# Kernel tuning notes

Measured on AMD Instinct MI355X. Metric: run time of the kernel, lower is better.

Reference implementation:

```python
import jax, jax.numpy as jnp
import numpy as np

N = 50000      # nodes per type
E = 800000     # edges per relation
CIN = 64       # in_channels
H, O = 2, 32   # heads, out_channels
HID = H * O    # hidden
EC = 16        # edge_channels


def setup_inputs() -> dict:
    key = jax.random.key(0)
    ks = jax.random.split(key, 30)
    f = lambda i, shape, s=0.1: jax.random.normal(ks[i], shape, dtype=jnp.float32) * s
    inp = {
        'x_a': f(0, (N, CIN), 1.0), 'x_b': f(1, (N, CIN), 1.0),
        'edge_attr1': f(2, (E, EC), 1.0), 'edge_attr2': f(3, (E, EC), 1.0),
        'Wq_a': f(4, (CIN, HID)), 'Wk_a': f(5, (CIN, HID)), 'Wv_a': f(6, (CIN, HID)),
        'Wq_b': f(7, (CIN, HID)), 'Wk_b': f(8, (CIN, HID)), 'Wv_b': f(9, (CIN, HID)),
        'emb_a': f(10, (HID,)), 'emb_b': f(11, (HID,)),
        'rel1': f(12, (HID,)), 'rel2': f(13, (HID,)),
        'We': f(14, (EC, HID)), 'a_attn': f(15, (4 * O,)),
        'Wo_a': f(16, (HID, O)), 'bo_a': f(17, (O,)),
        'Wo_b': f(18, (HID, O)), 'bo_b': f(19, (O,)),
        'Wr_a': f(20, (CIN, O)), 'Wr_b': f(21, (CIN, O)),
        'row1': jax.random.randint(ks[22], (E,), 0, N),
        'col1': jax.random.randint(ks[23], (E,), 0, N),
        'row2': jax.random.randint(ks[24], (E,), 0, N),
        'col2': jax.random.randint(ks[25], (E,), 0, N),
    }
    return inp


def _edge_softmax(scores, col, num_dst):
    # softmax over incoming edges of each destination node; scores: [E, H]
    m = jax.ops.segment_max(scores, col, num_segments=num_dst)      # [N, H]
    ex = jnp.exp(scores - m[col])
    s = jax.ops.segment_sum(ex, col, num_segments=num_dst)          # [N, H]
    return ex / s[col]


def _relation(q_dst, k_src, v_src, emb_src, emb_dst, rel_emb, edge_bias,
              row, col, a_attn, num_dst):
    eb = edge_bias                                                  # [E, H, O]
    qd = q_dst[col] + emb_dst.reshape(1, H, O)
    ks = k_src[row] + emb_src.reshape(1, H, O)
    rb = jnp.broadcast_to(rel_emb.reshape(1, H, O), qd.shape)
    attn_in = jnp.concatenate([qd, ks, rb, eb], axis=-1)            # [E, H, 4O]
    scores = jnp.einsum('ehd,d->eh', jnp.tanh(attn_in), a_attn)    # [E, H]
    w = _edge_softmax(scores, col, num_dst)                         # [E, H]
    msg = v_src[row] + rel_emb.reshape(1, H, O) + eb                # [E, H, O]
    agg = jax.ops.segment_sum(msg * w[..., None], col, num_segments=num_dst)
    return agg.reshape(num_dst, H * O)


def reference(x_a, x_b, edge_attr1, edge_attr2,
              Wq_a, Wk_a, Wv_a, Wq_b, Wk_b, Wv_b,
              emb_a, emb_b, rel1, rel2, We, a_attn,
              Wo_a, bo_a, Wo_b, bo_b, Wr_a, Wr_b,
              row1, col1, row2, col2):
    q_a = (x_a @ Wq_a).reshape(-1, H, O)
    k_a = (x_a @ Wk_a).reshape(-1, H, O)
    v_a = (x_a @ Wv_a).reshape(-1, H, O)
    q_b = (x_b @ Wq_b).reshape(-1, H, O)
    k_b = (x_b @ Wk_b).reshape(-1, H, O)
    v_b = (x_b @ Wv_b).reshape(-1, H, O)

    # relation r1: a -> b
    eb1 = (edge_attr1 @ We).reshape(-1, H, O)
    out_b = _relation(q_b, k_a, v_a, emb_a, emb_b, rel1, eb1, row1, col1, a_attn, N)
    # relation r2: b -> a
    eb2 = (edge_attr2 @ We).reshape(-1, H, O)
    out_a = _relation(q_a, k_b, v_b, emb_b, emb_a, rel2, eb2, row2, col2, a_attn, N)

    fin_a = out_a @ Wo_a + bo_a + x_a @ Wr_a                        # [N, O]
    fin_b = out_b @ Wo_b + bo_b + x_b @ Wr_b                        # [N, O]
    return jnp.concatenate([fin_a, fin_b], axis=0)                  # [2N, O]
```

## Files before the change

### kernel.cpp

```cpp
#include <hip/hip_runtime.h>
#include <hip/hip_bf16.h>

typedef __hip_bfloat16 bf16;
typedef __attribute__((ext_vector_type(8))) short short8;
typedef __attribute__((ext_vector_type(4))) float float4v;

static __device__ __forceinline__ float b2f(bf16 x) { return __bfloat162float(x); }

static __device__ __forceinline__ float ldf(const void* p, size_t i, int f32) {
    return f32 ? ((const float*)p)[i] : b2f(((const bf16*)p)[i]);
}
static __device__ __forceinline__ void stf(void* p, size_t i, int f32, float v) {
    if (f32) ((float*)p)[i] = v;
    else     ((bf16*)p)[i] = __float2bfloat16(v);
}
static __device__ __forceinline__ unsigned short f2bf_bits(float f) {
    bf16 h = __float2bfloat16(f);
    return *(unsigned short*)&h;
}

static __device__ __forceinline__ float fast_tanh(float x) {
    float t = __expf(2.f * x);
    return 1.f - 2.f * __builtin_amdgcn_rcpf(t + 1.f);
}

__global__ void detect_kernel(const unsigned short* __restrict__ a, int* __restrict__ flag)
{
    __shared__ int cnt;
    if (threadIdx.x == 0) cnt = 0;
    __syncthreads();
    unsigned e = (a[threadIdx.x] >> 7) & 0xFF;
    if (e < 100 || e > 133) atomicAdd(&cnt, 1);
    __syncthreads();
    if (threadIdx.x == 0) *flag = (cnt >= 16) ? 1 : 0;
}

__global__ __launch_bounds__(256) void prep_small_kernel(
    const void* __restrict__ W0, const void* __restrict__ W1,
    const void* __restrict__ W2, const void* __restrict__ W3,
    const void* __restrict__ W4, const void* __restrict__ W5,
    const void* __restrict__ Wr_a, const void* __restrict__ Wr_b,
    const void* __restrict__ We,
    const void* __restrict__ Wo_a, const void* __restrict__ Wo_b,
    const void* __restrict__ rel1, const void* __restrict__ rel2,
    const void* __restrict__ a_attn, const int* __restrict__ flagp,
    unsigned short* __restrict__ wt,
    float* __restrict__ M1, float* __restrict__ c321,
    float* __restrict__ M2, float* __restrict__ c322,
    float* __restrict__ cvals)
{
    const int f32 = *flagp;
    const int bid = blockIdx.x;
    if (bid < 6) {
        const void* src;
        switch (bid) {
            case 0: src = W0; break; case 1: src = W1; break; case 2: src = W2; break;
            case 3: src = W3; break; case 4: src = W4; break; default: src = W5; break;
        }
        unsigned short* dst = wt + bid * 4096;
        for (int i = threadIdx.x; i < 4096; i += 256) {
            int c = i >> 6, j = i & 63;
            dst[j * 64 + c] = f2bf_bits(ldf(src, c * 64 + j, f32));
        }
    } else if (bid < 8) {
        const void* src = (bid == 6) ? Wr_a : Wr_b;
        unsigned short* dst = wt + 24576 + (bid - 6) * 2048;
        for (int i = threadIdx.x; i < 2048; i += 256) {
            int c = i >> 5, j = i & 31;
            dst[j * 64 + c] = f2bf_bits(ldf(src, c * 32 + j, f32));
        }
    } else if (bid < 10) {
        const int sel = bid - 8;
        const void* Wo  = sel ? Wo_a : Wo_b;
        const void* rel = sel ? rel2 : rel1;
        float* M   = sel ? M2 : M1;
        float* c32 = sel ? c322 : c321;
        const int t = threadIdx.x;
        for (int i = t; i < 1024; i += 256) {
            int m = i >> 5, j = i & 31;
            int h = m >> 4, c = m & 15;
            float s = 0.f;
            for (int jj = 0; jj < 32; ++jj)
                s += ldf(We, c * 64 + h * 32 + jj, f32) * ldf(Wo, (size_t)(h * 32 + jj) * 32 + j, f32);
            M[m * 32 + j] = s;
        }
        if (t < 32) {
            float s2 = 0.f;
            for (int ch = 0; ch < 64; ++ch)
                s2 += ldf(rel, ch, f32) * ldf(Wo, (size_t)ch * 32 + t, f32);
            c32[t] = s2;
        }
        if (t == 252 || t == 253) {
            int h = t - 252;
            float s3 = 0.f;
            for (int l = 0; l < 32; ++l)
                s3 += tanhf(ldf(rel, h * 32 + l, f32)) * ldf(a_attn, 64 + l, f32);
            cvals[sel * 2 + h] = s3;
        }
    } else {
        unsigned short* wet = wt + 28672;
        for (int i = threadIdx.x; i < 1024; i += 256) {
            int n = i >> 4, k = i & 15;
            wet[n * 16 + k] = f2bf_bits(ldf(We, k * 64 + n, f32));
        }
    }
}

__global__ __launch_bounds__(256) void node_prep_mfma_kernel(
    const void* __restrict__ x_a, const void* __restrict__ x_b,
    const unsigned short* __restrict__ wt,
    const void* __restrict__ emb_a, const void* __restrict__ emb_b,
    const void* __restrict__ a_attn, const int* __restrict__ flagp,
    unsigned short* __restrict__ v_a, unsigned short* __restrict__ v_b,
    float* __restrict__ r_a, float* __restrict__ r_b,
    float* __restrict__ sq_a, float* __restrict__ sk_a,
    float* __restrict__ sq_b, float* __restrict__ sk_b,
    const int* __restrict__ col1, const int* __restrict__ col2,
    int* __restrict__ cnt, int* __restrict__ rank_out,
    int n_nodes, int tiles, int mfma_blocks, int num_e)
{
    const int f32 = *flagp;

    if ((int)blockIdx.x >= mfma_blocks) {
        const int hb  = blockIdx.x - mfma_blocks;
        const int sel = hb & 1;
        const int bx  = hb >> 1;
        const int* col = sel ? col2 : col1;
        const int rb = sel ? n_nodes : 0;
        int e = bx * 256 + threadIdx.x;
        if (e < num_e)
            rank_out[(size_t)sel * num_e + e] = atomicAdd(&cnt[rb + col[e]], 1);
        return;
    }

    const int wave_id = blockIdx.x * 4 + (threadIdx.x >> 6);
    if (wave_id >= 2 * tiles) return;
    const int type = (wave_id >= tiles);
    const int tile = type ? (wave_id - tiles) : wave_id;

    const void* xp = type ? x_b : x_a;
    const unsigned short* wq = wt + (type ? 3 * 4096 : 0);
    const unsigned short* wk = wq + 4096;
    const unsigned short* wv = wk + 4096;
    const unsigned short* wr = wt + 24576 + (type ? 2048 : 0);
    const void* embp = type ? emb_b : emb_a;
    unsigned short* v_out = type ? v_b : v_a;
    float*  r_out  = type ? r_b : r_a;
    float2* sq_out = (float2*)(type ? sq_b : sq_a);
    float2* sk_out = (float2*)(type ? sk_b : sk_a);

    const int lane = threadIdx.x & 63;
    const int ml   = lane & 15;
    const int g    = lane >> 4;
    const int g8   = g * 8;

    float embc[4], acq[4], ack[4];
    #pragma unroll
    for (int t = 0; t < 4; ++t) {
        int colt = t * 16 + ml;
        embc[t] = ldf(embp, colt, f32);
        acq[t]  = ldf(a_attn, colt & 31, f32);
        ack[t]  = ldf(a_attn, 32 + (colt & 31), f32);
    }

    short8 Bq[4][2], Bk[4][2], Bv[4][2], Br[2][2];
    #pragma unroll
    for (int t = 0; t < 4; ++t) {
        const int rowo = (t * 16 + ml) * 64;
        #pragma unroll
        for (int kh = 0; kh < 2; ++kh) {
            const int o = rowo + kh * 32 + g8;
            Bq[t][kh] = __builtin_bit_cast(short8, *(const uint4*)(wq + o));
            Bk[t][kh] = __builtin_bit_cast(short8, *(const uint4*)(wk + o));
            Bv[t][kh] = __builtin_bit_cast(short8, *(const uint4*)(wv + o));
            if (t < 2)
                Br[t][kh] = __builtin_bit_cast(short8, *(const uint4*)(wr + o));
        }
    }

    const int n0 = tile << 4;
    int nr = n0 + ml; if (nr > n_nodes - 1) nr = n_nodes - 1;
    short8 A0, A1;
    if (f32) {
        const float4* xr = (const float4*)((const float*)xp + (size_t)nr * 64);
        float4 f0 = xr[2*g], f1 = xr[2*g+1], f2 = xr[8+2*g], f3 = xr[9+2*g];
        short8 a0, a1;
        a0[0]=(short)f2bf_bits(f0.x); a0[1]=(short)f2bf_bits(f0.y);
        a0[2]=(short)f2bf_bits(f0.z); a0[3]=(short)f2bf_bits(f0.w);
        a0[4]=(short)f2bf_bits(f1.x); a0[5]=(short)f2bf_bits(f1.y);
        a0[6]=(short)f2bf_bits(f1.z); a0[7]=(short)f2bf_bits(f1.w);
        a1[0]=(short)f2bf_bits(f2.x); a1[1]=(short)f2bf_bits(f2.y);
        a1[2]=(short)f2bf_bits(f2.z); a1[3]=(short)f2bf_bits(f2.w);
        a1[4]=(short)f2bf_bits(f3.x); a1[5]=(short)f2bf_bits(f3.y);
        a1[6]=(short)f2bf_bits(f3.z); a1[7]=(short)f2bf_bits(f3.w);
        A0 = a0; A1 = a1;
    } else {
        const uint4* xr = (const uint4*)((const bf16*)xp + (size_t)nr * 64);
        A0 = __builtin_bit_cast(short8, xr[g]);
        A1 = __builtin_bit_cast(short8, xr[4 + g]);
    }

    float4v accq[4], acck[4], accv[4], accr[2];
    #pragma unroll
    for (int t = 0; t < 4; ++t) {
        float4v z = {0.f, 0.f, 0.f, 0.f};
        accq[t] = z; acck[t] = z; accv[t] = z;
        if (t < 2) accr[t] = z;
    }
    #pragma unroll
    for (int t = 0; t < 4; ++t) {
        accq[t] = __builtin_amdgcn_mfma_f32_16x16x32_bf16(A0, Bq[t][0], accq[t], 0, 0, 0);
        accq[t] = __builtin_amdgcn_mfma_f32_16x16x32_bf16(A1, Bq[t][1], accq[t], 0, 0, 0);
        acck[t] = __builtin_amdgcn_mfma_f32_16x16x32_bf16(A0, Bk[t][0], acck[t], 0, 0, 0);
        acck[t] = __builtin_amdgcn_mfma_f32_16x16x32_bf16(A1, Bk[t][1], acck[t], 0, 0, 0);
        accv[t] = __builtin_amdgcn_mfma_f32_16x16x32_bf16(A0, Bv[t][0], accv[t], 0, 0, 0);
        accv[t] = __builtin_amdgcn_mfma_f32_16x16x32_bf16(A1, Bv[t][1], accv[t], 0, 0, 0);
        if (t < 2) {
            accr[t] = __builtin_amdgcn_mfma_f32_16x16x32_bf16(A0, Br[t][0], accr[t], 0, 0, 0);
            accr[t] = __builtin_amdgcn_mfma_f32_16x16x32_bf16(A1, Br[t][1], accr[t], 0, 0, 0);
        }
    }

    #pragma unroll
    for (int t = 0; t < 4; ++t) {
        #pragma unroll
        for (int r = 0; r < 4; ++r) {
            int node = n0 + g * 4 + r;
            if (node < n_nodes) {
                v_out[(size_t)node * 64 + t * 16 + ml] = f2bf_bits(accv[t][r]);
                if (t < 2) r_out[(size_t)node * 32 + t * 16 + ml] = accr[t][r];
            }
        }
    }

    #pragma unroll
    for (int r = 0; r < 4; ++r) {
        float q0 = fast_tanh(accq[0][r] + embc[0]) * acq[0]
                 + fast_tanh(accq[1][r] + embc[1]) * acq[1];
        float q1 = fast_tanh(accq[2][r] + embc[2]) * acq[2]
                 + fast_tanh(accq[3][r] + embc[3]) * acq[3];
        float k0 = fast_tanh(acck[0][r] + embc[0]) * ack[0]
                 + fast_tanh(acck[1][r] + embc[1]) * ack[1];
        float k1 = fast_tanh(acck[2][r] + embc[2]) * ack[2]
                 + fast_tanh(acck[3][r] + embc[3]) * ack[3];
        #pragma unroll
        for (int o = 1; o < 16; o <<= 1) {
            q0 += __shfl_xor(q0, o, 64); q1 += __shfl_xor(q1, o, 64);
            k0 += __shfl_xor(k0, o, 64); k1 += __shfl_xor(k1, o, 64);
        }
        int node = n0 + g * 4 + r;
        if (ml == 0 && node < n_nodes) {
            sq_out[node] = make_float2(q0, q1);
            sk_out[node] = make_float2(k0, k1);
        }
    }
}

__global__ __launch_bounds__(256) void scan1_kernel(const int* __restrict__ cnt,
                                                    int* __restrict__ partial, int n)
{
    __shared__ int wsum[4];
    int t = threadIdx.x;
    int i0 = blockIdx.x * 512 + 2 * t;
    int s = ((i0 < n) ? cnt[i0] : 0) + ((i0 + 1 < n) ? cnt[i0 + 1] : 0);
    #pragma unroll
    for (int o = 32; o; o >>= 1) s += __shfl_xor(s, o, 64);
    if ((t & 63) == 0) wsum[t >> 6] = s;
    __syncthreads();
    if (t == 0) partial[blockIdx.x] = wsum[0] + wsum[1] + wsum[2] + wsum[3];
}

__global__ void scan2_kernel(const int* __restrict__ partial, int* __restrict__ pp,
                             int* __restrict__ off, int nch, int noff)
{
    int lane = threadIdx.x;
    int running = 0;
    for (int base = 0; base < nch; base += 64) {
        int i = base + lane;
        int o = (i < nch) ? partial[i] : 0;
        int v = o;
        #pragma unroll
        for (int d = 1; d < 64; d <<= 1) {
            int u = __shfl_up(v, d, 64);
            if (lane >= d) v += u;
        }
        if (i < nch) pp[i] = running + v - o;
        running += __shfl(v, 63, 64);
    }
    if (lane == 0) off[noff] = running;
}

__global__ __launch_bounds__(256) void scan3_kernel(const int* __restrict__ cnt,
                                                    const int* __restrict__ pp,
                                                    int* __restrict__ off, int n)
{
    __shared__ int tmp[256];
    int t = threadIdx.x;
    int i0 = blockIdx.x * 512 + 2 * t;
    int v0 = (i0 < n) ? cnt[i0] : 0;
    int v1 = (i0 + 1 < n) ? cnt[i0 + 1] : 0;
    int pair = v0 + v1;
    tmp[t] = pair;
    __syncthreads();
    for (int d = 1; d < 256; d <<= 1) {
        int x = (t >= d) ? tmp[t - d] : 0;
        __syncthreads();
        tmp[t] += x;
        __syncthreads();
    }
    int excl = tmp[t] - pair + pp[blockIdx.x];
    if (i0 < n)     off[i0] = excl;
    if (i0 + 1 < n) off[i0 + 1] = excl + v0;
}

__global__ __launch_bounds__(256) void edge_score_scatter_kernel(
    const void* __restrict__ ea1p, const void* __restrict__ ea2p,
    const unsigned short* __restrict__ wet,
    const int* __restrict__ row1, const int* __restrict__ col1,
    const int* __restrict__ row2, const int* __restrict__ col2,
    const float* __restrict__ sq_bp, const float* __restrict__ sk_ap,
    const float* __restrict__ sq_ap, const float* __restrict__ sk_bp,
    const float* __restrict__ cvals, const void* __restrict__ a_attn,
    const int* __restrict__ flagp,
    const int* __restrict__ offs, const int* __restrict__ rankp,
    uint4* __restrict__ payload, int n_nodes, int num_e)
{
    const int f32 = *flagp;
    const int sel = blockIdx.x & 1;
    const int bx  = blockIdx.x >> 1;
    const void* ea = sel ? ea2p : ea1p;
    const int* row = sel ? row2 : row1;
    const int* col = sel ? col2 : col1;
    const float* sq_dst = sel ? sq_ap : sq_bp;
    const float* sk_src = sel ? sk_bp : sk_ap;
    const int rb = sel ? n_nodes : 0;
    const int* rankr = rankp + (size_t)sel * num_e;

    const int lane = threadIdx.x & 63;
    const int wv   = threadIdx.x >> 6;
    const int ml   = lane & 15;
    const int g    = lane >> 4;
    const int rsel = lane & 3;

    const int base = bx * 256 + wv * 64;
    if (base >= num_e) return;

    const short8 zero8 = {0, 0, 0, 0, 0, 0, 0, 0};

    short8 B[4];
    #pragma unroll
    for (int t = 0; t < 4; ++t)
        B[t] = (g < 2) ? __builtin_bit_cast(short8, *(const uint4*)(wet + (t * 16 + ml) * 16 + g * 8))
                       : zero8;
    float av[4];
    #pragma unroll
    for (int t = 0; t < 4; ++t) av[t] = ldf(a_attn, 96 + ((t * 16 + ml) & 31), f32);
    const float c0 = cvals[sel * 2 + 0];
    const float c1 = cvals[sel * 2 + 1];

    int pcol[4]; unsigned psrc[4]; int prank[4];
    #pragma unroll
    for (int it = 0; it < 4; ++it) { pcol[it] = 0; psrc[it] = 0; prank[it] = 0; }
    if (ml < 4) {
        #pragma unroll
        for (int it = 0; it < 4; ++it) {
            int e = base + it * 16 + g * 4 + rsel;
            int ec = (e < num_e) ? e : (num_e - 1);
            pcol[it]  = col[ec];
            psrc[it]  = (unsigned)row[ec];
            prank[it] = rankr[ec];
        }
    }

    short8 A[4];
    #pragma unroll
    for (int it = 0; it < 4; ++it) {
        int ec = base + it * 16 + ml; if (ec > num_e - 1) ec = num_e - 1;
        if (g < 2) {
            if (f32) {
                const float4* p = (const float4*)((const float*)ea + (size_t)ec * 16 + g * 8);
                float4 f0 = p[0], f1 = p[1];
                short8 a;
                a[0] = (short)f2bf_bits(f0.x); a[1] = (short)f2bf_bits(f0.y);
                a[2] = (short)f2bf_bits(f0.z); a[3] = (short)f2bf_bits(f0.w);
                a[4] = (short)f2bf_bits(f1.x); a[5] = (short)f2bf_bits(f1.y);
                a[6] = (short)f2bf_bits(f1.z); a[7] = (short)f2bf_bits(f1.w);
                A[it] = a;
            } else {
                A[it] = __builtin_bit_cast(short8, *(const uint4*)((const bf16*)ea + (size_t)ec * 16 + g * 8));
            }
        } else {
            A[it] = zero8;
        }
    }

    int ppos[4]; float2 psq[4], psk[4];
    #pragma unroll
    for (int it = 0; it < 4; ++it) {
        ppos[it] = 0;
        psq[it] = make_float2(0.f, 0.f); psk[it] = make_float2(0.f, 0.f);
    }
    if (ml < 4) {
        #pragma unroll
        for (int it = 0; it < 4; ++it) {
            psq[it] = ((const float2*)sq_dst)[pcol[it]];
            psk[it] = ((const float2*)sk_src)[psrc[it]];
            ppos[it] = offs[rb + pcol[it]] + prank[it];
        }
    }

    #pragma unroll
    for (int it = 0; it < 4; ++it) {
        const int e0 = base + it * 16;
        if (e0 < num_e) {
            float4v z = {0.f, 0.f, 0.f, 0.f};
            float4v acc0 = z, acc1 = z, acc2 = z, acc3 = z;
            acc0 = __builtin_amdgcn_mfma_f32_16x16x32_bf16(A[it], B[0], acc0, 0, 0, 0);
            acc1 = __builtin_amdgcn_mfma_f32_16x16x32_bf16(A[it], B[1], acc1, 0, 0, 0);
            acc2 = __builtin_amdgcn_mfma_f32_16x16x32_bf16(A[it], B[2], acc2, 0, 0, 0);
            acc3 = __builtin_amdgcn_mfma_f32_16x16x32_bf16(A[it], B[3], acc3, 0, 0, 0);

            float s0[4], s1[4];
            #pragma unroll
            for (int r = 0; r < 4; ++r) {
                s0[r] = fast_tanh(acc0[r]) * av[0] + fast_tanh(acc1[r]) * av[1];
                s1[r] = fast_tanh(acc2[r]) * av[2] + fast_tanh(acc3[r]) * av[3];
            }
            #pragma unroll
            for (int o = 1; o < 16; o <<= 1) {
                #pragma unroll
                for (int r = 0; r < 4; ++r) {
                    s0[r] += __shfl_xor(s0[r], o, 64);
                    s1[r] += __shfl_xor(s1[r], o, 64);
                }
            }

            const bool fin = (ml < 4) && (e0 + g * 4 + rsel < num_e);
            if (fin) {
                float a0 = (rsel == 0) ? s0[0] : (rsel == 1) ? s0[1] : (rsel == 2) ? s0[2] : s0[3];
                float a1 = (rsel == 0) ? s1[0] : (rsel == 1) ? s1[1] : (rsel == 2) ? s1[2] : s1[3];
                float v0 = fminf(30.f, fmaxf(-30.f, a0 + psq[it].x + psk[it].x + c0));
                float v1 = fminf(30.f, fmaxf(-30.f, a1 + psq[it].y + psk[it].y + c1));
                uint4* rec = payload + (size_t)3 * ppos[it];
                rec[0] = make_uint4(psrc[it], __float_as_uint(__expf(v0)),
                                    __float_as_uint(__expf(v1)), 0u);
            }
            const int srcl = ((lane & 12) << 2) | (lane & 3);
            const int posx = __shfl(ppos[it], srcl, 64);
            if (lane < 32 && (e0 + ml < num_e)) {
                uint4* rec = payload + (size_t)3 * posx;
                rec[1 + g] = __builtin_bit_cast(uint4, A[it]);
            }
        }
    }
}

__global__ __launch_bounds__(256) void agg_final_kernel(
    const uint4* __restrict__ payload, const int* __restrict__ off,
    const unsigned short* __restrict__ v_a, const unsigned short* __restrict__ v_b,
    const float* __restrict__ r_a, const float* __restrict__ r_b,
    const void* __restrict__ Wo_a, const void* __restrict__ Wo_b,
    const void* __restrict__ bo_a, const void* __restrict__ bo_b,
    const float* __restrict__ M1, const float* __restrict__ M2,
    const float* __restrict__ c321, const float* __restrict__ c322,
    const int* __restrict__ flagp, void* __restrict__ out,
    int n_nodes, int nbh)
{
    const int sel = blockIdx.x & 1;
    const int bx  = blockIdx.x >> 1;
    const unsigned short* v_src = sel ? v_b : v_a;
    const float* r_src = sel ? r_a : r_b;
    const void*  Wo    = sel ? Wo_a : Wo_b;
    const void*  bo    = sel ? bo_a : bo_b;
    const float* M     = sel ? M2 : M1;
    const float* c32   = sel ? c322 : c321;
    const int relbase  = sel ? n_nodes : 0;
    const size_t out_off = sel ? 0 : (size_t)n_nodes * 32;

    const int f32  = *flagp;
    const int lane = threadIdx.x & 63;
    const int wv   = threadIdx.x >> 6;
    const int j    = lane & 31;
    const int half = lane >> 5;
    const int c16  = lane & 15;
    const bool hi  = (lane >= 32);

    __shared__ float stage[4][96];

    float WoR[32], MR[16];
    const int cb = half * 32;
    #pragma unroll
    for (int cc = 0; cc < 32; ++cc)
        WoR[cc] = ldf(Wo, (size_t)(cb + cc) * 32 + j, f32);
    const int ub = half * 16;
    #pragma unroll
    for (int cc = 0; cc < 16; ++cc) MR[cc] = M[(ub + cc) * 32 + j];
    const float boR  = ldf(bo, j, f32);
    const float c32R = c32[j];

    const int stride = nbh * 4;
    const int iters  = (n_nodes + stride - 1) / stride;
    int d = bx * 4 + wv;

    int dd0 = (d < n_nodes) ? d : (n_nodes - 1);
    int b_c  = off[relbase + dd0];
    int en_c = off[relbase + dd0 + 1];
    float rv_c = r_src[(size_t)dd0 * 32 + j];

    for (int it = 0; it < iters; ++it, d += stride) {
        const bool valid = (d < n_nodes);
        const int dd  = valid ? d : (n_nodes - 1);

        int b_n = 0, en_n = 0; float rv_n = 0.f;
        if (it + 1 < iters) {
            int dn  = d + stride;
            int ddn = (dn < n_nodes) ? dn : (n_nodes - 1);
            b_n  = off[relbase + ddn];
            en_n = off[relbase + ddn + 1];
            rv_n = r_src[(size_t)ddn * 32 + j];
        }

        const int b   = __builtin_amdgcn_readfirstlane(b_c);
        const int en  = __builtin_amdgcn_readfirstlane(en_c);
        const int deg = en - b;
        const float rv = rv_c;

        float den0 = 0.f, den1 = 0.f, y = 0.f, ua = 0.f;
        int k = b;
        #pragma unroll 1
        for (; k + 8 <= en; k += 8) {
            uint4 m[8];
            #pragma unroll
            for (int q = 0; q < 8; ++q) m[q] = payload[(size_t)3 * (k + q)];
            float ev[8];
            #pragma unroll
            for (int q = 0; q < 8; ++q) {
                const unsigned short* pq = (const unsigned short*)(payload + (size_t)3 * (k + q) + 1);
                ev[q] = __uint_as_float((unsigned)pq[c16] << 16);
            }
            float vv[8];
            #pragma unroll
            for (int q = 0; q < 8; ++q)
                vv[q] = __uint_as_float((unsigned)v_src[(size_t)m[q].x * 64 + lane] << 16);
            #pragma unroll
            for (int q = 0; q < 8; ++q) {
                float e0 = __uint_as_float(m[q].y), e1 = __uint_as_float(m[q].z);
                den0 += e0; den1 += e1;
                float xw = hi ? e1 : e0;
                y  = fmaf(xw, vv[q], y);
                ua = fmaf(xw, ev[q], ua);
            }
        }
        #pragma unroll 1
        for (; k < en; ++k) {
            uint4 mm = payload[(size_t)3 * k];
            const unsigned short* pq = (const unsigned short*)(payload + (size_t)3 * k + 1);
            float evs = __uint_as_float((unsigned)pq[c16] << 16);
            float vvs = __uint_as_float((unsigned)v_src[(size_t)mm.x * 64 + lane] << 16);
            float e0 = __uint_as_float(mm.y), e1 = __uint_as_float(mm.z);
            den0 += e0; den1 += e1;
            float xw = hi ? e1 : e0;
            y  = fmaf(xw, vvs, y);
            ua = fmaf(xw, evs, ua);
        }

        float inv0 = (deg > 0) ? __builtin_amdgcn_rcpf(den0) : 0.f;
        float inv1 = (deg > 0) ? __builtin_amdgcn_rcpf(den1) : 0.f;
        const float invh = hi ? inv1 : inv0;
        y  *= invh;
        ua *= invh;

        float* st = stage[wv];
        st[lane] = y;
        if ((lane & 31) < 16) st[64 + half * 16 + c16] = ua;
        __asm__ volatile("s_waitcnt lgkmcnt(0)" ::: "memory");

        float acc = 0.f;
        #pragma unroll
        for (int cc = 0; cc < 32; ++cc)
            acc = fmaf(st[cb + cc], WoR[cc], acc);
        #pragma unroll
        for (int cc = 0; cc < 16; ++cc)
            acc = fmaf(st[64 + ub + cc], MR[cc], acc);

        float other = __shfl(acc, lane ^ 32, 64);
        if (valid && lane < 32) {
            float o = acc + other + boR + rv + ((deg > 0) ? c32R : 0.f);
            stf(out, out_off + (size_t)dd * 32 + j, f32, o);
        }
        __asm__ volatile("" ::: "memory");
        __builtin_amdgcn_wave_barrier();

        b_c = b_n; en_c = en_n; rv_c = rv_n;
    }
}

extern "C" void kernel_launch(void* const* d_in, const int* in_sizes, int n_in,
                              void* d_out, int out_size, void* d_ws, size_t ws_size,
                              hipStream_t stream)
{
    const void* x_a   = d_in[0];
    const void* x_b   = d_in[1];
    const void* ea1   = d_in[2];
    const void* ea2   = d_in[3];
    const void* Wq_a  = d_in[4];
    const void* Wk_a  = d_in[5];
    const void* Wv_a  = d_in[6];
    const void* Wq_b  = d_in[7];
    const void* Wk_b  = d_in[8];
    const void* Wv_b  = d_in[9];
    const void* emb_a = d_in[10];
    const void* emb_b = d_in[11];
    const void* rel1  = d_in[12];
    const void* rel2  = d_in[13];
    const void* We    = d_in[14];
    const void* a_at  = d_in[15];
    const void* Wo_a  = d_in[16];
    const void* bo_a  = d_in[17];
    const void* Wo_b  = d_in[18];
    const void* bo_b  = d_in[19];
    const void* Wr_a  = d_in[20];
    const void* Wr_b  = d_in[21];
    const int*  row1  = (const int*)d_in[22];
    const int*  col1  = (const int*)d_in[23];
    const int*  row2  = (const int*)d_in[24];
    const int*  col2  = (const int*)d_in[25];

    const int N = in_sizes[0] / 64;
    const int E = in_sizes[22];

    float* ws = (float*)d_ws;
    size_t off = 0;
    int*   flag = (int*)ws;        off += 64;
    unsigned short* v_a = (unsigned short*)(ws + off); off += (size_t)N * 32;
    unsigned short* v_b = (unsigned short*)(ws + off); off += (size_t)N * 32;
    float* r_a  = ws + off;        off += (size_t)N * 32;
    float* r_b  = ws + off;        off += (size_t)N * 32;
    float* sq_a = ws + off;        off += (size_t)N * 2;
    float* sk_a = ws + off;        off += (size_t)N * 2;
    float* sq_b = ws + off;        off += (size_t)N * 2;
    float* sk_b = ws + off;        off += (size_t)N * 2;
    float* cvals = ws + off;       off += 4;
    off = (off + 3) & ~(size_t)3;
    unsigned short* wt = (unsigned short*)(ws + off); off += 29696 / 2;
    float* M1   = ws + off;        off += 1024;
    float* c321 = ws + off;        off += 32;
    float* M2   = ws + off;        off += 1024;
    float* c322 = ws + off;        off += 32;
    int*   cnt    = (int*)(ws + off);  off += (size_t)2 * N;
    int*   offs   = (int*)(ws + off);  off += (size_t)2 * N + 2;
    int*   rankp  = (int*)(ws + off);  off += (size_t)2 * E;
    int*   partial = (int*)(ws + off); off += 512;
    int*   pp      = (int*)(ws + off); off += 512;
    off = (off + 3) & ~(size_t)3;
    uint4* payload = (uint4*)(ws + off); off += (size_t)2 * E * 12;

    const int tiles        = (N + 15) >> 4;
    const int mfma_blocks  = (2 * tiles + 3) / 4;
    const int eb_blocks    = (E + 255) / 256;
    const int score_blocks = (E + 255) / 256;
    const int nch          = (2 * N + 511) / 512;
    const int agg_half     = 4096;

    detect_kernel<<<1, 128, 0, stream>>>((const unsigned short*)a_at, flag);
    hipMemsetAsync(cnt, 0, (size_t)2 * N * sizeof(int), stream);

    prep_small_kernel<<<11, 256, 0, stream>>>(
        Wq_a, Wk_a, Wv_a, Wq_b, Wk_b, Wv_b, Wr_a, Wr_b,
        We, Wo_a, Wo_b, rel1, rel2, a_at, flag,
        wt, M1, c321, M2, c322, cvals);

    node_prep_mfma_kernel<<<mfma_blocks + 2 * eb_blocks, 256, 0, stream>>>(
        x_a, x_b, wt, emb_a, emb_b, a_at, flag,
        v_a, v_b, r_a, r_b, sq_a, sk_a, sq_b, sk_b,
        col1, col2, cnt, rankp, N, tiles, mfma_blocks, E);

    scan1_kernel<<<nch, 256, 0, stream>>>(cnt, partial, 2 * N);
    scan2_kernel<<<1, 64, 0, stream>>>(partial, pp, offs, nch, 2 * N);
    scan3_kernel<<<nch, 256, 0, stream>>>(cnt, pp, offs, 2 * N);

    edge_score_scatter_kernel<<<2 * score_blocks, 256, 0, stream>>>(
        ea1, ea2, wt + 28672, row1, col1, row2, col2,
        sq_b, sk_a, sq_a, sk_b, cvals, a_at, flag,
        offs, rankp, payload, N, E);

    agg_final_kernel<<<2 * agg_half, 256, 0, stream>>>(
        payload, offs, v_a, v_b, r_a, r_b, Wo_a, Wo_b, bo_a, bo_b,
        M1, M2, c321, c322, flag, d_out, N, agg_half);
}
```

Measured before the change: 525.3 us.

## Pad edge payload records to 64 bytes and read them with coalesced lane-wide loads

Each per-edge payload record grows from 48 to 64 bytes and is written as four full uint4 slots by cooperating lanes using shuffles, instead of scattered partial writes. In the aggregation kernel a wavefront now reads four whole records with one coalesced dword-per-lane load and pulls the source index, exp weights and edge features out with cross-lane shuffles, replacing many small per-edge loads. The aggregation grid is also halved. The cost is more payload memory traffic from padding and extra shuffle instructions per edge.

```diff
diff --git a/kernel.cpp b/kernel.cpp
--- a/kernel.cpp
+++ b/kernel.cpp
@@ -435,22 +435,33 @@
                 }
             }
 
+            float ex0v = 0.f, ex1v = 0.f;
             const bool fin = (ml < 4) && (e0 + g * 4 + rsel < num_e);
             if (fin) {
                 float a0 = (rsel == 0) ? s0[0] : (rsel == 1) ? s0[1] : (rsel == 2) ? s0[2] : s0[3];
                 float a1 = (rsel == 0) ? s1[0] : (rsel == 1) ? s1[1] : (rsel == 2) ? s1[2] : s1[3];
                 float v0 = fminf(30.f, fmaxf(-30.f, a0 + psq[it].x + psk[it].x + c0));
                 float v1 = fminf(30.f, fmaxf(-30.f, a1 + psq[it].y + psk[it].y + c1));
-                uint4* rec = payload + (size_t)3 * ppos[it];
-                rec[0] = make_uint4(psrc[it], __float_as_uint(__expf(v0)),
-                                    __float_as_uint(__expf(v1)), 0u);
+                ex0v = __expf(v0); ex1v = __expf(v1);
             }
+
             const int srcl = ((lane & 12) << 2) | (lane & 3);
             const int posx = __shfl(ppos[it], srcl, 64);
-            if (lane < 32 && (e0 + ml < num_e)) {
-                uint4* rec = payload + (size_t)3 * posx;
-                rec[1 + g] = __builtin_bit_cast(uint4, A[it]);
-            }
+            const unsigned psx = (unsigned)__shfl((int)psrc[it], srcl, 64);
+            const float e0x = __shfl(ex0v, srcl, 64);
+            const float e1x = __shfl(ex1v, srcl, 64);
+            uint4 Au = __builtin_bit_cast(uint4, A[it]);
+            uint4 Ad;
+            Ad.x = (unsigned)__shfl((int)Au.x, lane - 16, 64);
+            Ad.y = (unsigned)__shfl((int)Au.y, lane - 16, 64);
+            Ad.z = (unsigned)__shfl((int)Au.z, lane - 16, 64);
+            Ad.w = (unsigned)__shfl((int)Au.w, lane - 16, 64);
+            const int part = g;
+            uint4 data = (part == 0)
+                ? make_uint4(psx, __float_as_uint(e0x), __float_as_uint(e1x), 0u)
+                : (part < 3) ? Ad : make_uint4(0u, 0u, 0u, 0u);
+            if (e0 + ml < num_e)
+                payload[((size_t)posx << 2) + part] = data;
         }
     }
 }
@@ -484,6 +495,7 @@
     const int half = lane >> 5;
     const int c16  = lane & 15;
     const bool hi  = (lane >= 32);
+    const int ccs  = 4 + (c16 >> 1);
 
     __shared__ float stage[4][96];
 
@@ -497,6 +509,8 @@
     for (int cc = 0; cc < 16; ++cc) MR[cc] = M[(ub + cc) * 32 + j];
     const float boR  = ldf(bo, j, f32);
     const float c32R = c32[j];
+
+    const unsigned* payd = (const unsigned*)payload;
 
     const int stride = nbh * 4;
     const int iters  = (n_nodes + stride - 1) / stride;
@@ -529,39 +543,44 @@
         int k = b;
         #pragma unroll 1
         for (; k + 8 <= en; k += 8) {
-            uint4 m[8];
-            #pragma unroll
-            for (int q = 0; q < 8; ++q) m[q] = payload[(size_t)3 * (k + q)];
-            float ev[8];
-            #pragma unroll
-            for (int q = 0; q < 8; ++q) {
-                const unsigned short* pq = (const unsigned short*)(payload + (size_t)3 * (k + q) + 1);
-                ev[q] = __uint_as_float((unsigned)pq[c16] << 16);
-            }
+            unsigned w0 = payd[(size_t)k * 16 + lane];
+            unsigned w1 = payd[(size_t)(k + 4) * 16 + lane];
             float vv[8];
             #pragma unroll
-            for (int q = 0; q < 8; ++q)
-                vv[q] = __uint_as_float((unsigned)v_src[(size_t)m[q].x * 64 + lane] << 16);
+            for (int q = 0; q < 4; ++q) {
+                unsigned s0 = (unsigned)__shfl((int)w0, 16 * q, 64);
+                unsigned s1 = (unsigned)__shfl((int)w1, 16 * q, 64);
+                vv[q]     = __uint_as_float((unsigned)v_src[(size_t)s0 * 64 + lane] << 16);
+                vv[4 + q] = __uint_as_float((unsigned)v_src[(size_t)s1 * 64 + lane] << 16);
+            }
             #pragma unroll
-            for (int q = 0; q < 8; ++q) {
-                float e0 = __uint_as_float(m[q].y), e1 = __uint_as_float(m[q].z);
-                den0 += e0; den1 += e1;
-                float xw = hi ? e1 : e0;
-                y  = fmaf(xw, vv[q], y);
-                ua = fmaf(xw, ev[q], ua);
+            for (int h = 0; h < 2; ++h) {
+                unsigned wub = h ? w1 : w0;
+                #pragma unroll
+                for (int q = 0; q < 4; ++q) {
+                    float e0 = __uint_as_float((unsigned)__shfl((int)wub, 16 * q + 1, 64));
+                    float e1 = __uint_as_float((unsigned)__shfl((int)wub, 16 * q + 2, 64));
+                    unsigned ed = (unsigned)__shfl((int)wub, 16 * q + ccs, 64);
+                    float eav = __uint_as_float((c16 & 1) ? (ed & 0xffff0000u) : (ed << 16));
+                    den0 += e0; den1 += e1;
+                    float xw = hi ? e1 : e0;
+                    y  = fmaf(xw, vv[4 * h + q], y);
+                    ua = fmaf(xw, eav, ua);
+                }
             }
         }
         #pragma unroll 1
         for (; k < en; ++k) {
-            uint4 mm = payload[(size_t)3 * k];
-            const unsigned short* pq = (const unsigned short*)(payload + (size_t)3 * k + 1);
-            float evs = __uint_as_float((unsigned)pq[c16] << 16);
-            float vvs = __uint_as_float((unsigned)v_src[(size_t)mm.x * 64 + lane] << 16);
-            float e0 = __uint_as_float(mm.y), e1 = __uint_as_float(mm.z);
+            const uint4* rec = payload + ((size_t)k << 2);
+            uint4 m0 = rec[0];
+            const unsigned short* pq = (const unsigned short*)(rec + 1);
+            float eav = __uint_as_float((unsigned)pq[c16] << 16);
+            float vvs = __uint_as_float((unsigned)v_src[(size_t)m0.x * 64 + lane] << 16);
+            float e0 = __uint_as_float(m0.y), e1 = __uint_as_float(m0.z);
             den0 += e0; den1 += e1;
             float xw = hi ? e1 : e0;
             y  = fmaf(xw, vvs, y);
-            ua = fmaf(xw, evs, ua);
+            ua = fmaf(xw, eav, ua);
         }
 
         float inv0 = (deg > 0) ? __builtin_amdgcn_rcpf(den0) : 0.f;
@@ -652,15 +671,15 @@
     int*   rankp  = (int*)(ws + off);  off += (size_t)2 * E;
     int*   partial = (int*)(ws + off); off += 512;
     int*   pp      = (int*)(ws + off); off += 512;
-    off = (off + 3) & ~(size_t)3;
-    uint4* payload = (uint4*)(ws + off); off += (size_t)2 * E * 12;
+    off = (off + 15) & ~(size_t)15;
+    uint4* payload = (uint4*)(ws + off); off += (size_t)2 * E * 16;
 
     const int tiles        = (N + 15) >> 4;
     const int mfma_blocks  = (2 * tiles + 3) / 4;
     const int eb_blocks    = (E + 255) / 256;
     const int score_blocks = (E + 255) / 256;
     const int nch          = (2 * N + 511) / 512;
-    const int agg_half     = 4096;
+    const int agg_half     = 2048;
 
     detect_kernel<<<1, 128, 0, stream>>>((const unsigned short*)a_at, flag);
     hipMemsetAsync(cnt, 0, (size_t)2 * N * sizeof(int), stream);
```

Result: slower. 537.9 us (+2.4%).
